# Kernel optimization log

Measured on AMD Instinct MI355X. Metric: run time of the kernel, lower is better.

## Reference

```python
import jax, jax.numpy as jnp
import numpy as np

B, T, H = 64, 1024, 1024


def setup_inputs() -> dict:
    key = jax.random.key(0)
    ks = jax.random.split(key, 8)
    s = 1.0 / np.sqrt(H)
    return {
        "spatial_feats": jax.random.normal(ks[0], (B, T, H), dtype=jnp.float32),
        "hidden_state": jax.random.normal(ks[1], (B, H), dtype=jnp.float32),
        "W_enc": jax.random.uniform(ks[2], (H, H), jnp.float32, -s, s),
        "b_enc": jax.random.uniform(ks[3], (H,), jnp.float32, -s, s),
        "W_dec": jax.random.uniform(ks[4], (H, H), jnp.float32, -s, s),
        "b_dec": jax.random.uniform(ks[5], (H,), jnp.float32, -s, s),
        "w_score": jax.random.uniform(ks[6], (H,), jnp.float32, -s, s),
        "b_score": jax.random.uniform(ks[7], (), jnp.float32, -s, s),
    }


def reference(spatial_feats, hidden_state, W_enc, b_enc, W_dec, b_dec, w_score, b_score):
    # decoder_proj(hidden_state): [B, H] -> [B, 1, H]
    dec = (jnp.einsum("bh,oh->bo", hidden_state, W_dec) + b_dec)[:, None, :]
    # encoder_proj(spatial_feats): [B, T, H]
    enc = jnp.einsum("bth,oh->bto", spatial_feats, W_enc) + b_enc
    energy = jnp.tanh(enc + dec)                      # [B, T, H]
    scores = jnp.einsum("bth,h->bt", energy, w_score) + b_score  # [B, T]
    weights = jax.nn.softmax(scores, axis=1)          # [B, T]
    context = jnp.einsum("bth,bt->bh", spatial_feats, weights)   # [B, H]
    return (context, weights)
```

## Files before the change

kernel.cpp:

```cpp
#include <hip/hip_runtime.h>
#include <hip/hip_bf16.h>
#include <math.h>


typedef __attribute__((ext_vector_type(8))) short bf16x8;
typedef __attribute__((ext_vector_type(4))) float f32x4;

__device__ __forceinline__ unsigned short f2bf(float f) {
  union { float f; unsigned int u; } v; v.f = f;
  unsigned int r = v.u + 0x7FFFu + ((v.u >> 16) & 1u);
  return (unsigned short)(r >> 16);
}

__device__ __forceinline__ float fast_tanh(float x) {
  float e = __expf(2.0f * x);
  return 1.0f - 2.0f / (e + 1.0f);
}

__device__ __forceinline__ void gld16(const void* g, void* l) {
  __builtin_amdgcn_global_load_lds(
      (const __attribute__((address_space(1))) void*)g,
      (__attribute__((address_space(3))) void*)l, 16, 0, 0);
}

__global__ __launch_bounds__(256) void prep_kernel(
    const float* __restrict__ spatial, const float* __restrict__ hidden,
    const float* __restrict__ W_enc, const float* __restrict__ b_enc,
    const float* __restrict__ W_dec, const float* __restrict__ b_dec,
    unsigned short* __restrict__ Wbf, unsigned short* __restrict__ Abf,
    float* __restrict__ dec, float* __restrict__ scores, int nW, int nA) {
  __shared__ float hs[1024];
  const int bid = blockIdx.x, tid = threadIdx.x;
  if (bid < nW + nA) {
    const float* src = (bid < nW) ? W_enc : spatial;
    unsigned short* dst = (bid < nW) ? Wbf : Abf;
    size_t g4 = (size_t)(bid < nW ? bid : bid - nW) * 256 + tid;
    float4 v = ((const float4*)src)[g4];
    ushort4 o;
    o.x = f2bf(v.x); o.y = f2bf(v.y); o.z = f2bf(v.z); o.w = f2bf(v.w);
    *(ushort4*)(dst + g4 * 4) = o;
    return;
  }
  const int dbid = bid - nW - nA;
  const int b = dbid >> 3, o0 = (dbid & 7) * 128;
  const int wave = tid >> 6, lane = tid & 63;
  int gid = dbid * 256 + tid;
  if (gid < 65536) scores[gid] = 0.f;
  ((float4*)hs)[tid] = ((const float4*)(hidden + (size_t)b * 1024))[tid];
  __syncthreads();
  for (int it = 0; it < 32; it++) {
    int o = o0 + it * 4 + wave;
    const float4* w4 = (const float4*)(W_dec + (size_t)o * 1024);
    float4 acc; acc.x = acc.y = acc.z = acc.w = 0.f;
    #pragma unroll
    for (int j = 0; j < 4; j++) {
      int i = j * 64 + lane;
      float4 x = ((const float4*)hs)[i], y = w4[i];
      acc.x = fmaf(x.x, y.x, acc.x);
      acc.y = fmaf(x.y, y.y, acc.y);
      acc.z = fmaf(x.z, y.z, acc.z);
      acc.w = fmaf(x.w, y.w, acc.w);
    }
    float v = (acc.x + acc.y) + (acc.z + acc.w);
    #pragma unroll
    for (int off = 1; off < 64; off <<= 1) v += __shfl_xor(v, off);
    if (lane == 0) dec[b * 1024 + o] = v + b_dec[o] + b_enc[o];
  }
}

__global__ __launch_bounds__(256) void enc_score_bf16_kernel(
    const unsigned short* __restrict__ A,
    const unsigned short* __restrict__ W,
    const float* __restrict__ dec,
    const float* __restrict__ w_score,
    float* __restrict__ scores)
{
  __shared__ unsigned short As[2][128 * 32];
  __shared__ unsigned short Bs[2][128 * 32];

  const int bid = blockIdx.x;
  const int n0 = (bid & 7) * 128;
  const int m0 = (bid >> 3) * 128;
  const int tid = threadIdx.x;
  const int lane = tid & 63, wave = tid >> 6;
  const int wm = (wave >> 1) * 64, wn = (wave & 1) * 64;
  const int quad = lane >> 4, colL = lane & 15;

  const int srow = wave * 32 + (lane >> 2);
  const int scol = (lane & 3) * 8;
  const unsigned short* ga = A + (size_t)(m0 + srow) * 1024 + scol;
  const unsigned short* gb = W + (size_t)(n0 + srow) * 1024 + scol;
  const int lbase0 = wave * 32 * 32 + lane * 8;

  f32x4 acc[4][4];
  #pragma unroll
  for (int mi = 0; mi < 4; mi++)
    #pragma unroll
    for (int ni = 0; ni < 4; ni++)
      acc[mi][ni] = (f32x4){0.f, 0.f, 0.f, 0.f};

  for (int k0 = 0; k0 < 1024; k0 += 64) {
    #pragma unroll
    for (int kh = 0; kh < 2; kh++) {
      #pragma unroll
      for (int j = 0; j < 2; j++) {
        int goff = k0 + kh * 32 + j * 16 * 1024;
        int loff = lbase0 + j * 16 * 32;
        gld16(ga + goff, &As[kh][loff]);
        gld16(gb + goff, &Bs[kh][loff]);
      }
    }
    __syncthreads();
    #pragma unroll
    for (int kh = 0; kh < 2; kh++) {
      bf16x8 af[4], bfr[4];
      #pragma unroll
      for (int i = 0; i < 4; i++) {
        af[i]  = *(const bf16x8*)(&As[kh][(wm + i * 16 + colL) * 32 + quad * 8]);
        bfr[i] = *(const bf16x8*)(&Bs[kh][(wn + i * 16 + colL) * 32 + quad * 8]);
      }
      #pragma unroll
      for (int mi = 0; mi < 4; mi++)
        #pragma unroll
        for (int ni = 0; ni < 4; ni++)
          acc[mi][ni] = __builtin_amdgcn_mfma_f32_16x16x32_bf16(
              af[mi], bfr[ni], acc[mi][ni], 0, 0, 0);
    }
    __syncthreads();
  }

  const int b = m0 >> 10;
  float decv[4], wsv[4];
  #pragma unroll
  for (int ni = 0; ni < 4; ni++) {
    int n = n0 + wn + ni * 16 + colL;
    decv[ni] = dec[b * 1024 + n];
    wsv[ni] = w_score[n];
  }
  #pragma unroll
  for (int mi = 0; mi < 4; mi++) {
    float rs[4] = {0.f, 0.f, 0.f, 0.f};
    #pragma unroll
    for (int ni = 0; ni < 4; ni++)
      #pragma unroll
      for (int r = 0; r < 4; r++)
        rs[r] += fast_tanh(acc[mi][ni][r] + decv[ni]) * wsv[ni];
    #pragma unroll
    for (int r = 0; r < 4; r++) {
      float v = rs[r];
      v += __shfl_xor(v, 1);
      v += __shfl_xor(v, 2);
      v += __shfl_xor(v, 4);
      v += __shfl_xor(v, 8);
      if (colL == 0)
        atomicAdd(&scores[m0 + wm + mi * 16 + quad * 4 + r], v);
    }
  }
}

__global__ __launch_bounds__(256) void enc_score_f32_kernel(
    const float* __restrict__ A, const float* __restrict__ W,
    const float* __restrict__ dec, const float* __restrict__ w_score,
    float* __restrict__ scores) {
  __shared__ unsigned short As[128][32];
  __shared__ unsigned short Bs[128][32];
  const int bid = blockIdx.x;
  const int n0 = (bid & 7) * 128;
  const int m0 = (bid >> 3) * 128;
  const int tid = threadIdx.x;
  const int lane = tid & 63, wave = tid >> 6;
  const int wm = (wave >> 1) * 64, wn = (wave & 1) * 64;
  const int quad = lane >> 4, colL = lane & 15;
  const int srow = tid >> 3;
  const int scol = (tid & 7) * 4;
  f32x4 acc[4][4];
  #pragma unroll
  for (int mi = 0; mi < 4; mi++)
    #pragma unroll
    for (int ni = 0; ni < 4; ni++)
      acc[mi][ni] = (f32x4){0.f, 0.f, 0.f, 0.f};
  for (int k0 = 0; k0 < 1024; k0 += 32) {
    #pragma unroll
    for (int p = 0; p < 4; p++) {
      int r = p * 32 + srow;
      float4 va = *(const float4*)(A + (size_t)(m0 + r) * 1024 + (k0 + scol));
      float4 vb = *(const float4*)(W + (size_t)(n0 + r) * 1024 + (k0 + scol));
      ushort4 pa, pb;
      pa.x = f2bf(va.x); pa.y = f2bf(va.y); pa.z = f2bf(va.z); pa.w = f2bf(va.w);
      pb.x = f2bf(vb.x); pb.y = f2bf(vb.y); pb.z = f2bf(vb.z); pb.w = f2bf(vb.w);
      *(ushort4*)(&As[r][scol]) = pa;
      *(ushort4*)(&Bs[r][scol]) = pb;
    }
    __syncthreads();
    bf16x8 af[4], bfr[4];
    #pragma unroll
    for (int i = 0; i < 4; i++) {
      af[i]  = *(const bf16x8*)(&As[wm + i * 16 + colL][quad * 8]);
      bfr[i] = *(const bf16x8*)(&Bs[wn + i * 16 + colL][quad * 8]);
    }
    #pragma unroll
    for (int mi = 0; mi < 4; mi++)
      #pragma unroll
      for (int ni = 0; ni < 4; ni++)
        acc[mi][ni] = __builtin_amdgcn_mfma_f32_16x16x32_bf16(
            af[mi], bfr[ni], acc[mi][ni], 0, 0, 0);
    __syncthreads();
  }
  const int b = m0 >> 10;
  float decv[4], wsv[4];
  #pragma unroll
  for (int ni = 0; ni < 4; ni++) {
    int n = n0 + wn + ni * 16 + colL;
    decv[ni] = dec[b * 1024 + n];
    wsv[ni] = w_score[n];
  }
  #pragma unroll
  for (int mi = 0; mi < 4; mi++) {
    float rs[4] = {0.f, 0.f, 0.f, 0.f};
    #pragma unroll
    for (int ni = 0; ni < 4; ni++)
      #pragma unroll
      for (int r = 0; r < 4; r++)
        rs[r] += fast_tanh(acc[mi][ni][r] + decv[ni]) * wsv[ni];
    #pragma unroll
    for (int r = 0; r < 4; r++) {
      float v = rs[r];
      v += __shfl_xor(v, 1);
      v += __shfl_xor(v, 2);
      v += __shfl_xor(v, 4);
      v += __shfl_xor(v, 8);
      if (colL == 0)
        atomicAdd(&scores[m0 + wm + mi * 16 + quad * 4 + r], v);
    }
  }
}

__global__ void softmax_kernel(const float* __restrict__ scores,
                               float* __restrict__ weights,
                               float* __restrict__ context) {
  __shared__ float red[256];
  int b = blockIdx.x, tid = threadIdx.x;
  float4 z; z.x = z.y = z.z = z.w = 0.f;
  ((float4*)context)[blockIdx.x * 256 + tid] = z;
  const float* s = scores + b * 1024;
  float v[4];
  float mx = -1e30f;
  #pragma unroll
  for (int i = 0; i < 4; i++) { v[i] = s[tid + i * 256]; mx = fmaxf(mx, v[i]); }
  red[tid] = mx; __syncthreads();
  for (int off = 128; off > 0; off >>= 1) {
    if (tid < off) red[tid] = fmaxf(red[tid], red[tid + off]);
    __syncthreads();
  }
  mx = red[0]; __syncthreads();
  float sum = 0.f;
  #pragma unroll
  for (int i = 0; i < 4; i++) { v[i] = __expf(v[i] - mx); sum += v[i]; }
  red[tid] = sum; __syncthreads();
  for (int off = 128; off > 0; off >>= 1) {
    if (tid < off) red[tid] += red[tid + off];
    __syncthreads();
  }
  float inv = 1.0f / red[0];
  #pragma unroll
  for (int i = 0; i < 4; i++) weights[b * 1024 + tid + i * 256] = v[i] * inv;
}

__global__ void context_kernel(const float* __restrict__ spatial,
                               const float* __restrict__ weights,
                               float* __restrict__ context) {
  int b = blockIdx.x >> 3, tq = blockIdx.x & 7;
  int tid = threadIdx.x;
  __shared__ float wl[128];
  if (tid < 128) wl[tid] = weights[b * 1024 + tq * 128 + tid];
  __syncthreads();
  const float4* sp =
      (const float4*)(spatial + ((size_t)(b * 1024 + tq * 128)) * 1024);
  float4 acc; acc.x = acc.y = acc.z = acc.w = 0.f;
  #pragma unroll 4
  for (int t = 0; t < 128; t++) {
    float w = wl[t];
    float4 x = sp[(size_t)t * 256 + tid];
    acc.x = fmaf(w, x.x, acc.x);
    acc.y = fmaf(w, x.y, acc.y);
    acc.z = fmaf(w, x.z, acc.z);
    acc.w = fmaf(w, x.w, acc.w);
  }
  float* c = context + b * 1024 + tid * 4;
  atomicAdd(c + 0, acc.x);
  atomicAdd(c + 1, acc.y);
  atomicAdd(c + 2, acc.z);
  atomicAdd(c + 3, acc.w);
}

extern "C" void kernel_launch(void* const* d_in, const int* in_sizes, int n_in,
                              void* d_out, int out_size, void* d_ws, size_t ws_size,
                              hipStream_t stream) {
  const float* spatial  = (const float*)d_in[0];
  const float* hidden   = (const float*)d_in[1];
  const float* W_enc    = (const float*)d_in[2];
  const float* b_enc    = (const float*)d_in[3];
  const float* W_dec    = (const float*)d_in[4];
  const float* b_dec    = (const float*)d_in[5];
  const float* w_score  = (const float*)d_in[6];

  float* out      = (float*)d_out;
  float* context  = out;
  float* weights  = out + 65536;

  float* scores   = (float*)d_ws;
  float* dec      = scores + 65536;
  unsigned short* Wbf = (unsigned short*)(dec + 65536);
  unsigned short* Abf = Wbf + 1024 * 1024;

  const size_t need = 512 * 1024 + 2ull * 1024 * 1024 + 2ull * 65536 * 1024;

  if (ws_size >= need) {
    const int nW = 1024, nA = 65536;
    prep_kernel<<<nW + nA + 512, 256, 0, stream>>>(
        spatial, hidden, W_enc, b_enc, W_dec, b_dec, Wbf, Abf, dec, scores,
        nW, nA);
    enc_score_bf16_kernel<<<4096, 256, 0, stream>>>(Abf, Wbf, dec, w_score,
                                                    scores);
  } else {
    prep_kernel<<<512, 256, 0, stream>>>(
        spatial, hidden, W_enc, b_enc, W_dec, b_dec, nullptr, nullptr, dec,
        scores, 0, 0);
    enc_score_f32_kernel<<<4096, 256, 0, stream>>>(spatial, W_enc, dec,
                                                   w_score, scores);
  }

  softmax_kernel<<<64, 256, 0, stream>>>(scores, weights, context);
  context_kernel<<<512, 256, 0, stream>>>(spatial, weights, context);
}
```

Before: 688.3 us.

## Loop over N tiles per block, write partial scores, read bf16 in context

Result: faster. 672.4 us (-2.3%).

```diff
diff --git a/kernel.cpp b/kernel.cpp
--- a/kernel.cpp
+++ b/kernel.cpp
@@ -4,12 +4,18 @@
 
 
 typedef __attribute__((ext_vector_type(8))) short bf16x8;
+typedef __attribute__((ext_vector_type(8))) unsigned short ushort8;
 typedef __attribute__((ext_vector_type(4))) float f32x4;
 
 __device__ __forceinline__ unsigned short f2bf(float f) {
   union { float f; unsigned int u; } v; v.f = f;
   unsigned int r = v.u + 0x7FFFu + ((v.u >> 16) & 1u);
   return (unsigned short)(r >> 16);
+}
+
+__device__ __forceinline__ float bf2f(unsigned short b) {
+  union { unsigned int u; float f; } v; v.u = ((unsigned int)b) << 16;
+  return v.f;
 }
 
 __device__ __forceinline__ float fast_tanh(float x) {
@@ -28,7 +34,7 @@
     const float* __restrict__ W_enc, const float* __restrict__ b_enc,
     const float* __restrict__ W_dec, const float* __restrict__ b_dec,
     unsigned short* __restrict__ Wbf, unsigned short* __restrict__ Abf,
-    float* __restrict__ dec, float* __restrict__ scores, int nW, int nA) {
+    float* __restrict__ dec, int nW, int nA) {
   __shared__ float hs[1024];
   const int bid = blockIdx.x, tid = threadIdx.x;
   if (bid < nW + nA) {
@@ -44,8 +50,6 @@
   const int dbid = bid - nW - nA;
   const int b = dbid >> 3, o0 = (dbid & 7) * 128;
   const int wave = tid >> 6, lane = tid & 63;
-  int gid = dbid * 256 + tid;
-  if (gid < 65536) scores[gid] = 0.f;
   ((float4*)hs)[tid] = ((const float4*)(hidden + (size_t)b * 1024))[tid];
   __syncthreads();
   for (int it = 0; it < 32; it++) {
@@ -73,14 +77,15 @@
     const unsigned short* __restrict__ W,
     const float* __restrict__ dec,
     const float* __restrict__ w_score,
-    float* __restrict__ scores)
+    float* __restrict__ scores_p)
 {
-  __shared__ unsigned short As[2][128 * 32];
-  __shared__ unsigned short Bs[2][128 * 32];
+  __shared__ unsigned short As[128 * 32];
+  __shared__ unsigned short Bs[128 * 32];
 
   const int bid = blockIdx.x;
-  const int n0 = (bid & 7) * 128;
-  const int m0 = (bid >> 3) * 128;
+  const int m_tile = (bid >> 4) * 8 + (bid & 7);
+  const int nh = (bid >> 3) & 1;
+  const int m0 = m_tile * 128;
   const int tid = threadIdx.x;
   const int lane = tid & 63, wave = tid >> 6;
   const int wm = (wave >> 1) * 64, wn = (wave & 1) * 64;
@@ -89,35 +94,38 @@
   const int srow = wave * 32 + (lane >> 2);
   const int scol = (lane & 3) * 8;
   const unsigned short* ga = A + (size_t)(m0 + srow) * 1024 + scol;
-  const unsigned short* gb = W + (size_t)(n0 + srow) * 1024 + scol;
-  const int lbase0 = wave * 32 * 32 + lane * 8;
-
-  f32x4 acc[4][4];
+  unsigned short* la = As + wave * 1024;
+  unsigned short* lb = Bs + wave * 1024;
+
+  const int b = m0 >> 10;
+  float rs[4][4];
   #pragma unroll
   for (int mi = 0; mi < 4; mi++)
     #pragma unroll
-    for (int ni = 0; ni < 4; ni++)
-      acc[mi][ni] = (f32x4){0.f, 0.f, 0.f, 0.f};
-
-  for (int k0 = 0; k0 < 1024; k0 += 64) {
-    #pragma unroll
-    for (int kh = 0; kh < 2; kh++) {
-      #pragma unroll
-      for (int j = 0; j < 2; j++) {
-        int goff = k0 + kh * 32 + j * 16 * 1024;
-        int loff = lbase0 + j * 16 * 32;
-        gld16(ga + goff, &As[kh][loff]);
-        gld16(gb + goff, &Bs[kh][loff]);
-      }
-    }
-    __syncthreads();
-    #pragma unroll
-    for (int kh = 0; kh < 2; kh++) {
+    for (int r = 0; r < 4; r++) rs[mi][r] = 0.f;
+
+  for (int nt = 0; nt < 4; nt++) {
+    const int n0 = (nh * 4 + nt) * 128;
+    const unsigned short* gb = W + (size_t)(n0 + srow) * 1024 + scol;
+
+    f32x4 acc[4][4];
+    #pragma unroll
+    for (int mi = 0; mi < 4; mi++)
+      #pragma unroll
+      for (int ni = 0; ni < 4; ni++)
+        acc[mi][ni] = (f32x4){0.f, 0.f, 0.f, 0.f};
+
+    for (int k0 = 0; k0 < 1024; k0 += 32) {
+      gld16(ga + k0,             la);
+      gld16(ga + k0 + 16 * 1024, la + 512);
+      gld16(gb + k0,             lb);
+      gld16(gb + k0 + 16 * 1024, lb + 512);
+      __syncthreads();
       bf16x8 af[4], bfr[4];
       #pragma unroll
       for (int i = 0; i < 4; i++) {
-        af[i]  = *(const bf16x8*)(&As[kh][(wm + i * 16 + colL) * 32 + quad * 8]);
-        bfr[i] = *(const bf16x8*)(&Bs[kh][(wn + i * 16 + colL) * 32 + quad * 8]);
+        af[i]  = *(const bf16x8*)(As + (wm + i * 16 + colL) * 32 + quad * 8);
+        bfr[i] = *(const bf16x8*)(Bs + (wn + i * 16 + colL) * 32 + quad * 8);
       }
       #pragma unroll
       for (int mi = 0; mi < 4; mi++)
@@ -125,43 +133,44 @@
         for (int ni = 0; ni < 4; ni++)
           acc[mi][ni] = __builtin_amdgcn_mfma_f32_16x16x32_bf16(
               af[mi], bfr[ni], acc[mi][ni], 0, 0, 0);
-    }
-    __syncthreads();
-  }
-
-  const int b = m0 >> 10;
-  float decv[4], wsv[4];
-  #pragma unroll
-  for (int ni = 0; ni < 4; ni++) {
-    int n = n0 + wn + ni * 16 + colL;
-    decv[ni] = dec[b * 1024 + n];
-    wsv[ni] = w_score[n];
-  }
-  #pragma unroll
-  for (int mi = 0; mi < 4; mi++) {
-    float rs[4] = {0.f, 0.f, 0.f, 0.f};
-    #pragma unroll
-    for (int ni = 0; ni < 4; ni++)
-      #pragma unroll
-      for (int r = 0; r < 4; r++)
-        rs[r] += fast_tanh(acc[mi][ni][r] + decv[ni]) * wsv[ni];
+      __syncthreads();
+    }
+
+    float decv[4], wsv[4];
+    #pragma unroll
+    for (int ni = 0; ni < 4; ni++) {
+      int n = n0 + wn + ni * 16 + colL;
+      decv[ni] = dec[b * 1024 + n];
+      wsv[ni] = w_score[n];
+    }
+    #pragma unroll
+    for (int mi = 0; mi < 4; mi++)
+      #pragma unroll
+      for (int ni = 0; ni < 4; ni++)
+        #pragma unroll
+        for (int r = 0; r < 4; r++)
+          rs[mi][r] += fast_tanh(acc[mi][ni][r] + decv[ni]) * wsv[ni];
+  }
+
+  const int slot = nh * 2 + (wave & 1);
+  #pragma unroll
+  for (int mi = 0; mi < 4; mi++)
     #pragma unroll
     for (int r = 0; r < 4; r++) {
-      float v = rs[r];
+      float v = rs[mi][r];
       v += __shfl_xor(v, 1);
       v += __shfl_xor(v, 2);
       v += __shfl_xor(v, 4);
       v += __shfl_xor(v, 8);
       if (colL == 0)
-        atomicAdd(&scores[m0 + wm + mi * 16 + quad * 4 + r], v);
-    }
-  }
+        scores_p[slot * 65536 + m0 + wm + mi * 16 + quad * 4 + r] = v;
+    }
 }
 
 __global__ __launch_bounds__(256) void enc_score_f32_kernel(
     const float* __restrict__ A, const float* __restrict__ W,
     const float* __restrict__ dec, const float* __restrict__ w_score,
-    float* __restrict__ scores) {
+    float* __restrict__ scores_p) {
   __shared__ unsigned short As[128][32];
   __shared__ unsigned short Bs[128][32];
   const int bid = blockIdx.x;
@@ -216,37 +225,41 @@
   }
   #pragma unroll
   for (int mi = 0; mi < 4; mi++) {
-    float rs[4] = {0.f, 0.f, 0.f, 0.f};
+    float rsv[4] = {0.f, 0.f, 0.f, 0.f};
     #pragma unroll
     for (int ni = 0; ni < 4; ni++)
       #pragma unroll
       for (int r = 0; r < 4; r++)
-        rs[r] += fast_tanh(acc[mi][ni][r] + decv[ni]) * wsv[ni];
+        rsv[r] += fast_tanh(acc[mi][ni][r] + decv[ni]) * wsv[ni];
     #pragma unroll
     for (int r = 0; r < 4; r++) {
-      float v = rs[r];
+      float v = rsv[r];
       v += __shfl_xor(v, 1);
       v += __shfl_xor(v, 2);
       v += __shfl_xor(v, 4);
       v += __shfl_xor(v, 8);
       if (colL == 0)
-        atomicAdd(&scores[m0 + wm + mi * 16 + quad * 4 + r], v);
-    }
-  }
-}
-
-__global__ void softmax_kernel(const float* __restrict__ scores,
+        atomicAdd(&scores_p[m0 + wm + mi * 16 + quad * 4 + r], v);
+    }
+  }
+}
+
+__global__ void softmax_kernel(const float* __restrict__ scores_p,
                                float* __restrict__ weights,
                                float* __restrict__ context) {
   __shared__ float red[256];
   int b = blockIdx.x, tid = threadIdx.x;
   float4 z; z.x = z.y = z.z = z.w = 0.f;
   ((float4*)context)[blockIdx.x * 256 + tid] = z;
-  const float* s = scores + b * 1024;
   float v[4];
   float mx = -1e30f;
   #pragma unroll
-  for (int i = 0; i < 4; i++) { v[i] = s[tid + i * 256]; mx = fmaxf(mx, v[i]); }
+  for (int i = 0; i < 4; i++) {
+    int m = b * 1024 + tid + i * 256;
+    v[i] = scores_p[m] + scores_p[65536 + m] + scores_p[2 * 65536 + m] +
+           scores_p[3 * 65536 + m];
+    mx = fmaxf(mx, v[i]);
+  }
   red[tid] = mx; __syncthreads();
   for (int off = 128; off > 0; off >>= 1) {
     if (tid < off) red[tid] = fmaxf(red[tid], red[tid + off]);
@@ -266,9 +279,48 @@
   for (int i = 0; i < 4; i++) weights[b * 1024 + tid + i * 256] = v[i] * inv;
 }
 
-__global__ void context_kernel(const float* __restrict__ spatial,
-                               const float* __restrict__ weights,
-                               float* __restrict__ context) {
+__global__ void context_bf16_kernel(const unsigned short* __restrict__ Abf,
+                                    const float* __restrict__ weights,
+                                    float* __restrict__ context) {
+  int b = blockIdx.x >> 3, tq = blockIdx.x & 7;
+  int tid = threadIdx.x;
+  __shared__ float wl[128];
+  __shared__ float cs[128 * 8];
+  if (tid < 128) wl[tid] = weights[b * 1024 + tq * 128 + tid];
+  __syncthreads();
+  const int hl = tid & 127, p = tid >> 7;
+  const int h0 = hl * 8;
+  const unsigned short* sp =
+      Abf + ((size_t)(b * 1024 + tq * 128 + p)) * 1024 + h0;
+  float acc[8];
+  #pragma unroll
+  for (int j = 0; j < 8; j++) acc[j] = 0.f;
+  for (int t = 0; t < 128; t += 2) {
+    float w = wl[t + p];
+    ushort8 x = *(const ushort8*)(sp + (size_t)t * 1024);
+    #pragma unroll
+    for (int j = 0; j < 8; j++) acc[j] = fmaf(w, bf2f(x[j]), acc[j]);
+  }
+  if (p == 0) {
+    #pragma unroll
+    for (int j = 0; j < 8; j++) cs[hl * 8 + j] = acc[j];
+  }
+  __syncthreads();
+  if (p == 1) {
+    #pragma unroll
+    for (int j = 0; j < 8; j++) cs[hl * 8 + j] += acc[j];
+  }
+  __syncthreads();
+  if (p == 0) {
+    #pragma unroll
+    for (int j = 0; j < 8; j++)
+      atomicAdd(&context[b * 1024 + h0 + j], cs[hl * 8 + j]);
+  }
+}
+
+__global__ void context_f32_kernel(const float* __restrict__ spatial,
+                                   const float* __restrict__ weights,
+                                   float* __restrict__ context) {
   int b = blockIdx.x >> 3, tq = blockIdx.x & 7;
   int tid = threadIdx.x;
   __shared__ float wl[128];
@@ -308,28 +360,30 @@
   float* context  = out;
   float* weights  = out + 65536;
 
-  float* scores   = (float*)d_ws;
-  float* dec      = scores + 65536;
+  float* scores_p = (float*)d_ws;
+  float* dec      = scores_p + 4 * 65536;
   unsigned short* Wbf = (unsigned short*)(dec + 65536);
   unsigned short* Abf = Wbf + 1024 * 1024;
 
-  const size_t need = 512 * 1024 + 2ull * 1024 * 1024 + 2ull * 65536 * 1024;
+  const size_t need =
+      4ull * 65536 * 4 + 65536 * 4 + 2ull * 1024 * 1024 + 2ull * 65536 * 1024;
 
   if (ws_size >= need) {
     const int nW = 1024, nA = 65536;
     prep_kernel<<<nW + nA + 512, 256, 0, stream>>>(
-        spatial, hidden, W_enc, b_enc, W_dec, b_dec, Wbf, Abf, dec, scores,
-        nW, nA);
-    enc_score_bf16_kernel<<<4096, 256, 0, stream>>>(Abf, Wbf, dec, w_score,
-                                                    scores);
+        spatial, hidden, W_enc, b_enc, W_dec, b_dec, Wbf, Abf, dec, nW, nA);
+    enc_score_bf16_kernel<<<1024, 256, 0, stream>>>(Abf, Wbf, dec, w_score,
+                                                    scores_p);
+    softmax_kernel<<<64, 256, 0, stream>>>(scores_p, weights, context);
+    context_bf16_kernel<<<512, 256, 0, stream>>>(Abf, weights, context);
   } else {
+    hipMemsetAsync(scores_p, 0, 4 * 65536 * sizeof(float), stream);
     prep_kernel<<<512, 256, 0, stream>>>(
         spatial, hidden, W_enc, b_enc, W_dec, b_dec, nullptr, nullptr, dec,
-        scores, 0, 0);
+        0, 0);
     enc_score_f32_kernel<<<4096, 256, 0, stream>>>(spatial, W_enc, dec,
-                                                   w_score, scores);
-  }
-
-  softmax_kernel<<<64, 256, 0, stream>>>(scores, weights, context);
-  context_kernel<<<512, 256, 0, stream>>>(spatial, weights, context);
-}
+                                                   w_score, scores_p);
+    softmax_kernel<<<64, 256, 0, stream>>>(scores_p, weights, context);
+    context_f32_kernel<<<512, 256, 0, stream>>>(spatial, weights, context);
+  }
+}
```
